# Kernel optimization log

Measured on AMD Instinct MI355X. Metric: run time of the kernel, lower is better.

The kernel has to match this reference:

```python
import jax, jax.numpy as jnp
import numpy as np

D_QK = 64

def _xavier(key, shape):
    # matches nn.init.xavier_uniform_ on (H, fan_in, fan_out)
    fan_in, fan_out = shape[-2], shape[-1]
    limit = float(np.sqrt(6.0 / (fan_in + fan_out)))
    return jax.random.uniform(key, shape, jnp.float32, -limit, limit)

def setup_inputs() -> dict:
    key = jax.random.key(0)
    kx, kq, kk, kv = jax.random.split(key, 4)
    B, M, d_model, H, d_QK, d_V = 4, 2048, 1024, 16, 64, 64
    x = jax.random.normal(kx, (B, M, d_model), jnp.float32)
    W_Q = _xavier(kq, (H, d_model, d_QK))
    W_K = _xavier(kk, (H, d_model, d_QK))
    W_V = _xavier(kv, (H, d_model, d_V))
    return {"x": x, "W_Q": W_Q, "W_K": W_K, "W_V": W_V}

def reference(x, W_Q, W_K, W_V):
    B, M, N = x.shape
    H = W_Q.shape[0]
    # per-head projections: [B,H,M,d]
    Q = jnp.einsum('bmn,hnd->bhmd', x, W_Q)
    K = jnp.einsum('bmn,hnd->bhmd', x, W_K)
    V = jnp.einsum('bmn,hnd->bhmd', x, W_V)
    scale = 1.0 / jnp.sqrt(jnp.asarray(D_QK, x.dtype))
    attn = jax.nn.softmax(jnp.einsum('bhmd,bhkd->bhmk', Q, K) * scale, axis=-1)
    out = jnp.einsum('bhmk,bhkd->bhmd', attn, V)  # [B,H,M,d_V]
    # transpose heads next to d_V and concat: [B,M,H*d_V] == [B,M,N]
    return out.transpose(0, 2, 1, 3).reshape(B, M, N)
```

## Files before the change

### kernel.cpp

```cpp
#include <hip/hip_runtime.h>

typedef __attribute__((ext_vector_type(8))) _Float16 f16x8;
typedef __attribute__((ext_vector_type(2))) __fp16 fp16v2;
typedef __attribute__((ext_vector_type(4))) float f32x4;
typedef _Float16 f16;
typedef unsigned short u16;
typedef unsigned int u32;

#define DEV __device__ __forceinline__

DEV u32 packh2(float a, float b) {
  union { f16 h[2]; u32 u; } x;
  x.h[0] = (f16)a; x.h[1] = (f16)b;
  return x.u;
}
DEV u32 pkrtz(float a, float b) {
  union { fp16v2 h; u32 u; } x;
  x.h = __builtin_amdgcn_cvt_pkrtz(a, b);
  return x.u;
}
DEV float exp2_fast(float x) {
  float r;
  asm("v_exp_f32 %0, %1" : "=v"(r) : "v"(x));
  return r;
}

typedef __attribute__((address_space(1))) const u32 ASG_u32;
typedef __attribute__((address_space(3))) u32 ASL_u32;
DEV void gload16(const void* g, void* l) {
  __builtin_amdgcn_global_load_lds((ASG_u32*)g, (ASL_u32*)l, 16, 0, 0);
}

__global__ __launch_bounds__(256) void k_half_x(const float* __restrict__ x,
                                                f16* __restrict__ xh) {
  const size_t i = ((size_t)blockIdx.x * 256 + threadIdx.x) * 8;
  float4 a = *(const float4*)(x + i);
  float4 c = *(const float4*)(x + i + 4);
  uint4 u;
  u.x = packh2(a.x, a.y); u.y = packh2(a.z, a.w);
  u.z = packh2(c.x, c.y); u.w = packh2(c.z, c.w);
  *(uint4*)(xh + i) = u;
}

__global__ __launch_bounds__(256) void k_prep_w(const float* __restrict__ Wq,
                                                const float* __restrict__ Wk,
                                                const float* __restrict__ Wv,
                                                f16* __restrict__ wt) {
  __shared__ float tile[64][65];
  const int bx = blockIdx.x;
  const int w = bx >> 8;
  const int rem = bx & 255;
  const int h = rem >> 4;
  const int nc = rem & 15;
  const float* W = (w == 0) ? Wq : ((w == 1) ? Wk : Wv);
  const int t = threadIdx.x;

  {
    const int r = t >> 2;
    const int cc = (t & 3) * 16;
    const float* src = W + ((size_t)h * 1024 + nc * 64 + r) * 64 + cc;
#pragma unroll
    for (int j = 0; j < 4; ++j) {
      float4 v = *(const float4*)(src + j * 4);
      tile[r][cc + j * 4 + 0] = v.x;
      tile[r][cc + j * 4 + 1] = v.y;
      tile[r][cc + j * 4 + 2] = v.z;
      tile[r][cc + j * 4 + 3] = v.w;
    }
  }
  __syncthreads();
  {
    const int d = t >> 2;
    const int n0 = (t & 3) * 16;
    const size_t base = ((size_t)(w * 16 + h) * 64 + d) * 1024 + nc * 64 + n0;
    uint4 u0, u1;
    u0.x = packh2(tile[n0 + 0][d], tile[n0 + 1][d]);
    u0.y = packh2(tile[n0 + 2][d], tile[n0 + 3][d]);
    u0.z = packh2(tile[n0 + 4][d], tile[n0 + 5][d]);
    u0.w = packh2(tile[n0 + 6][d], tile[n0 + 7][d]);
    u1.x = packh2(tile[n0 + 8][d], tile[n0 + 9][d]);
    u1.y = packh2(tile[n0 + 10][d], tile[n0 + 11][d]);
    u1.z = packh2(tile[n0 + 12][d], tile[n0 + 13][d]);
    u1.w = packh2(tile[n0 + 14][d], tile[n0 + 15][d]);
    *(uint4*)(wt + base) = u0;
    *(uint4*)(wt + base + 8) = u1;
  }
}

__global__ __launch_bounds__(256, 4) void k_proj(
    const f16* __restrict__ xh, const f16* __restrict__ wt,
    f16* __restrict__ Q, f16* __restrict__ K, f16* __restrict__ Vt) {
  __shared__ __align__(16) char ldsb[32768];
  int bid = blockIdx.x;
  bid = (bid & 7) * 192 + (bid >> 3);
  const int bm = bid / 24;
  const int bn = bid % 24;
  const int w = bn >> 3;
  const int hp = bn & 7;
  const int wrow = w * 1024 + hp * 128;
  const bool isV = (w == 2);
  const int t = threadIdx.x;
  const int wave = t >> 6;
  const int lane = t & 63;
  const int l15 = lane & 15;
  const int wr = wave >> 1;
  const int wc = wave & 1;

  f32x4 acc[4][4];
#pragma unroll
  for (int mi = 0; mi < 4; ++mi)
#pragma unroll
    for (int ni = 0; ni < 4; ++ni) acc[mi][ni] = (f32x4)(0.0f);

  for (int kt = 0; kt < 16; ++kt) {
    const int k0 = kt * 64;
#pragma unroll
    for (int i = 0; i < 4; ++i) {
      const int ci = wave * 4 + i;
      const int row = ci * 8 + (lane >> 3);
      const int cb = ((lane & 7) * 16) ^ ((row & 7) << 4);
      const size_t ga = ((size_t)(bm * 128 + row) * 1024 + k0) * 2;
      gload16((const char*)xh + ga + cb, ldsb + ci * 1024);
      const size_t gb = ((size_t)(wrow + row) * 1024 + k0) * 2;
      gload16((const char*)wt + gb + cb, ldsb + 16384 + ci * 1024);
    }
    __syncthreads();

#pragma unroll
    for (int ks = 0; ks < 2; ++ks) {
      f16x8 af[4], bfr[4];
#pragma unroll
      for (int mi = 0; mi < 4; ++mi) {
        const int row = wr * 64 + mi * 16 + l15;
        const int cb = (((lane >> 4) * 16) + ks * 64) ^ ((row & 7) << 4);
        af[mi] = *(const f16x8*)(ldsb + row * 128 + cb);
      }
#pragma unroll
      for (int ni = 0; ni < 4; ++ni) {
        const int row = wc * 64 + ni * 16 + l15;
        const int cb = (((lane >> 4) * 16) + ks * 64) ^ ((row & 7) << 4);
        bfr[ni] = *(const f16x8*)(ldsb + 16384 + row * 128 + cb);
      }
#pragma unroll
      for (int mi = 0; mi < 4; ++mi)
#pragma unroll
        for (int ni = 0; ni < 4; ++ni)
          acc[mi][ni] = __builtin_amdgcn_mfma_f32_16x16x32_f16(af[mi], bfr[ni], acc[mi][ni], 0, 0, 0);
    }
    __syncthreads();
  }

  const int rb = bm * 128 + wr * 64;
#pragma unroll
  for (int mi = 0; mi < 4; ++mi) {
#pragma unroll
    for (int ni = 0; ni < 4; ++ni) {
      f32x4 v = acc[mi][ni];
      const int dl = wc * 64 + ni * 16 + l15;
      const int hh = hp * 2 + (dl >> 6);
      const int d = dl & 63;
      const int m0 = rb + mi * 16 + ((lane >> 4) << 2);
      const int b = m0 >> 11;
      const int ml = m0 & 2047;
      if (isV) {
        uint2 u;
        u.x = packh2(v[0], v[1]);
        u.y = packh2(v[2], v[3]);
        *(uint2*)(Vt + ((size_t)((b * 16 + hh) * 64 + d)) * 2048 + ml) = u;
      } else {
        const float sc = (w == 0) ? 0.18033688f : 1.0f;
        f16* A = (w == 0) ? Q : K;
#pragma unroll
        for (int j = 0; j < 4; ++j)
          A[((size_t)(b * 16 + hh) * 2048 + (ml + j)) * 64 + d] = (f16)(v[j] * sc);
      }
    }
  }
}

__global__ __launch_bounds__(512, 4) void k_attn(
    const f16* __restrict__ Q, const f16* __restrict__ K,
    const f16* __restrict__ Vt, float* __restrict__ out) {
  __shared__ __align__(16) char ldsb[81920];
  const int raw = blockIdx.x;
  const int bh = (raw & 7) * 8 + (raw >> 6);
  const int qt = (raw >> 3) & 7;
  const int b = bh >> 4;
  const int h = bh & 15;
  const int t = threadIdx.x;
  const int wave = t >> 6;
  const int lane = t & 63;
  const int l15 = lane & 15;
  const int g = lane >> 4;
  char* sP = ldsb + 49152 + wave * 4096;

  f16x8 qf[2][2];
  const size_t qbase = ((size_t)bh * 2048 + qt * 256 + wave * 32) * 64;
#pragma unroll
  for (int mf = 0; mf < 2; ++mf)
#pragma unroll
    for (int ks = 0; ks < 2; ++ks) {
      const size_t off = qbase + (size_t)(mf * 16 + l15) * 64 + ks * 32 + g * 8;
      qf[mf][ks] = *(const f16x8*)(Q + off);
    }

  f32x4 o[2][4];
  float ms[2], ls[2];
#pragma unroll
  for (int mf = 0; mf < 2; ++mf) { ms[mf] = -1e30f; ls[mf] = 0.0f; }
#pragma unroll
  for (int mf = 0; mf < 2; ++mf)
#pragma unroll
    for (int df = 0; df < 4; ++df) o[mf][df] = (f32x4)(0.0f);

  const size_t kvbase = (size_t)bh * 2048 * 64;

  const int srow = wave * 8 + (lane >> 3);
  const int scb0 = ((lane & 7) * 16) ^ (((lane >> 3) & 7) << 4);

  auto stage = [&](int tile, int bufi) {
    char* dst = ldsb + bufi * 16384;
    const size_t gk = (kvbase + (size_t)(tile * 64 + srow) * 64) * 2;
    gload16((const char*)K + gk + scb0, dst + wave * 1024);
    const size_t gv = (kvbase + (size_t)srow * 2048 + tile * 64) * 2;
    gload16((const char*)Vt + gv + scb0, dst + 8192 + wave * 1024);
  };

  stage(0, 0);
  stage(1, 1);

  int cur = 0;
  int stg = 2;

#pragma unroll 1
  for (int ct = 0; ct < 32; ++ct) {
    if (ct < 31) {
      asm volatile("s_waitcnt vmcnt(2) lgkmcnt(0)" ::: "memory");
    } else {
      asm volatile("s_waitcnt vmcnt(0) lgkmcnt(0)" ::: "memory");
    }
    __builtin_amdgcn_s_barrier();
    __builtin_amdgcn_sched_barrier(0);

    if (ct + 2 < 32) stage(ct + 2, stg);

    const char* kb = ldsb + cur * 16384;
    const char* vbuf = kb + 8192;

    f32x4 st[2][4];
#pragma unroll
    for (int mf = 0; mf < 2; ++mf)
#pragma unroll
      for (int nf = 0; nf < 4; ++nf) st[mf][nf] = (f32x4)(0.0f);
#pragma unroll
    for (int ks = 0; ks < 2; ++ks) {
      f16x8 kf[4];
#pragma unroll
      for (int nf = 0; nf < 4; ++nf) {
        const int row = nf * 16 + l15;
        const int cb = ((g * 16) + ks * 64) ^ ((row & 7) << 4);
        kf[nf] = *(const f16x8*)(kb + row * 128 + cb);
      }
#pragma unroll
      for (int mf = 0; mf < 2; ++mf)
#pragma unroll
        for (int nf = 0; nf < 4; ++nf)
          st[mf][nf] = __builtin_amdgcn_mfma_f32_16x16x32_f16(kf[nf], qf[mf][ks], st[mf][nf], 0, 0, 0);
    }

#pragma unroll
    for (int mf = 0; mf < 2; ++mf) {
      float rm = fmaxf(fmaxf(fmaxf(st[mf][0][0], st[mf][0][1]), fmaxf(st[mf][0][2], st[mf][0][3])),
                       fmaxf(fmaxf(st[mf][1][0], st[mf][1][1]), fmaxf(st[mf][1][2], st[mf][1][3])));
      rm = fmaxf(rm, fmaxf(fmaxf(fmaxf(st[mf][2][0], st[mf][2][1]), fmaxf(st[mf][2][2], st[mf][2][3])),
                           fmaxf(fmaxf(st[mf][3][0], st[mf][3][1]), fmaxf(st[mf][3][2], st[mf][3][3]))));
      rm = fmaxf(rm, __shfl_xor(rm, 16));
      rm = fmaxf(rm, __shfl_xor(rm, 32));
      if (__any(rm > ms[mf] + 11.5f)) {
        const float mnew = fmaxf(ms[mf], rm);
        const float alpha = exp2_fast(ms[mf] - mnew);
        ms[mf] = mnew;
        ls[mf] *= alpha;
        f32x4 av;
#pragma unroll
        for (int j = 0; j < 4; ++j) av[j] = __shfl(alpha, g * 4 + j);
#pragma unroll
        for (int df = 0; df < 4; ++df) o[mf][df] *= av;
      }
      const float m = ms[mf];
      float p[4][4], part = 0.0f;
#pragma unroll
      for (int nf = 0; nf < 4; ++nf) {
#pragma unroll
        for (int j = 0; j < 4; ++j) {
          p[nf][j] = exp2_fast(st[mf][nf][j] - m);
          part += p[nf][j];
        }
      }
      ls[mf] += part;
      const int prow = mf * 16 + l15;
      char* pr = sP + prow * 128;
      const int swz = (prow & 7) << 4;
#pragma unroll
      for (int nf = 0; nf < 4; ++nf) {
        uint2 u;
        u.x = pkrtz(p[nf][0], p[nf][1]);
        u.y = pkrtz(p[nf][2], p[nf][3]);
        *(uint2*)(pr + (((nf << 5) + (g << 3)) ^ swz)) = u;
      }
    }
    asm volatile("" ::: "memory");

#pragma unroll
    for (int ks = 0; ks < 2; ++ks) {
      f16x8 pa[2];
#pragma unroll
      for (int mf = 0; mf < 2; ++mf) {
        const int prow = mf * 16 + l15;
        pa[mf] = *(const f16x8*)(sP + prow * 128 + ((ks * 64 + g * 16) ^ ((prow & 7) << 4)));
      }
#pragma unroll
      for (int df = 0; df < 4; ++df) {
        const int row = df * 16 + l15;
        const int cb = ((g * 16) + ks * 64) ^ ((row & 7) << 4);
        const f16x8 vb = *(const f16x8*)(vbuf + row * 128 + cb);
#pragma unroll
        for (int mf = 0; mf < 2; ++mf)
          o[mf][df] = __builtin_amdgcn_mfma_f32_16x16x32_f16(pa[mf], vb, o[mf][df], 0, 0, 0);
      }
    }

    cur = (cur == 2) ? 0 : cur + 1;
    stg = (stg == 2) ? 0 : stg + 1;
  }

#pragma unroll
  for (int mf = 0; mf < 2; ++mf) {
    float l = ls[mf];
    l += __shfl_xor(l, 16);
    l += __shfl_xor(l, 32);
    const float inv = 1.0f / l;
    f32x4 iv;
#pragma unroll
    for (int j = 0; j < 4; ++j) iv[j] = __shfl(inv, g * 4 + j);
#pragma unroll
    for (int j = 0; j < 4; ++j) {
      const int m = qt * 256 + wave * 32 + mf * 16 + g * 4 + j;
#pragma unroll
      for (int df = 0; df < 4; ++df) {
        const int d = df * 16 + l15;
        out[((size_t)(b * 2048 + m)) * 1024 + h * 64 + d] = o[mf][df][j] * iv[j];
      }
    }
  }
}

extern "C" void kernel_launch(void* const* d_in, const int* in_sizes, int n_in,
                              void* d_out, int out_size, void* d_ws, size_t ws_size,
                              hipStream_t stream) {
  (void)in_sizes; (void)n_in; (void)out_size; (void)ws_size;
  const float* x  = (const float*)d_in[0];
  const float* Wq = (const float*)d_in[1];
  const float* Wk = (const float*)d_in[2];
  const float* Wv = (const float*)d_in[3];
  float* out = (float*)d_out;

  f16* ws = (f16*)d_ws;
  f16* xh = ws + 0;
  f16* wt = ws + 8388608;
  f16* Q  = ws + 11534336;
  f16* K  = ws + 19922944;
  f16* Vt = ws + 28311552;

  k_half_x<<<4096, 256, 0, stream>>>(x, xh);
  k_prep_w<<<768, 256, 0, stream>>>(Wq, Wk, Wv, wt);
  k_proj<<<1536, 256, 0, stream>>>(xh, wt, Q, K, Vt);
  k_attn<<<512, 512, 0, stream>>>(Q, K, Vt, out);
}
```

Baseline: 183.1 us.

## Double per-wave query rows in attention and merge x/W prep kernels

The attention kernel now runs 4 waves per block, each handling 64 query rows instead of 32, with 8 waves before. Each K/V fragment read from LDS is reused across twice as many MFMAs, and each wave issues two async staging loads per tile. The x-to-half conversion and weight transpose kernels are merged into one launch to save a kernel launch. The cost is higher register pressure from doubled accumulators and fewer waves per block to hide latency.

```diff
diff --git a/kernel.cpp b/kernel.cpp
--- a/kernel.cpp
+++ b/kernel.cpp
@@ -31,29 +31,31 @@
   __builtin_amdgcn_global_load_lds((ASG_u32*)g, (ASL_u32*)l, 16, 0, 0);
 }
 
-__global__ __launch_bounds__(256) void k_half_x(const float* __restrict__ x,
-                                                f16* __restrict__ xh) {
-  const size_t i = ((size_t)blockIdx.x * 256 + threadIdx.x) * 8;
-  float4 a = *(const float4*)(x + i);
-  float4 c = *(const float4*)(x + i + 4);
-  uint4 u;
-  u.x = packh2(a.x, a.y); u.y = packh2(a.z, a.w);
-  u.z = packh2(c.x, c.y); u.w = packh2(c.z, c.w);
-  *(uint4*)(xh + i) = u;
-}
-
-__global__ __launch_bounds__(256) void k_prep_w(const float* __restrict__ Wq,
-                                                const float* __restrict__ Wk,
-                                                const float* __restrict__ Wv,
-                                                f16* __restrict__ wt) {
+__global__ __launch_bounds__(256) void k_pre(const float* __restrict__ x,
+                                             const float* __restrict__ Wq,
+                                             const float* __restrict__ Wk,
+                                             const float* __restrict__ Wv,
+                                             f16* __restrict__ xh,
+                                             f16* __restrict__ wt) {
   __shared__ float tile[64][65];
-  const int bx = blockIdx.x;
+  const int bx0 = blockIdx.x;
+  const int t = threadIdx.x;
+  if (bx0 < 4096) {
+    const size_t i = ((size_t)bx0 * 256 + t) * 8;
+    float4 a = *(const float4*)(x + i);
+    float4 c = *(const float4*)(x + i + 4);
+    uint4 u;
+    u.x = packh2(a.x, a.y); u.y = packh2(a.z, a.w);
+    u.z = packh2(c.x, c.y); u.w = packh2(c.z, c.w);
+    *(uint4*)(xh + i) = u;
+    return;
+  }
+  const int bx = bx0 - 4096;
   const int w = bx >> 8;
   const int rem = bx & 255;
   const int h = rem >> 4;
   const int nc = rem & 15;
   const float* W = (w == 0) ? Wq : ((w == 1) ? Wk : Wv);
-  const int t = threadIdx.x;
 
   {
     const int r = t >> 2;
@@ -178,7 +180,7 @@
   }
 }
 
-__global__ __launch_bounds__(512, 4) void k_attn(
+__global__ __launch_bounds__(256, 2) void k_attn(
     const f16* __restrict__ Q, const f16* __restrict__ K,
     const f16* __restrict__ Vt, float* __restrict__ out) {
   __shared__ __align__(16) char ldsb[81920];
@@ -192,38 +194,43 @@
   const int lane = t & 63;
   const int l15 = lane & 15;
   const int g = lane >> 4;
-  char* sP = ldsb + 49152 + wave * 4096;
-
-  f16x8 qf[2][2];
-  const size_t qbase = ((size_t)bh * 2048 + qt * 256 + wave * 32) * 64;
-#pragma unroll
-  for (int mf = 0; mf < 2; ++mf)
+  char* sP = ldsb + 49152 + wave * 8192;
+
+  f16x8 qf[4][2];
+  const size_t qbase = ((size_t)bh * 2048 + qt * 256 + wave * 64) * 64;
+#pragma unroll
+  for (int mf = 0; mf < 4; ++mf)
 #pragma unroll
     for (int ks = 0; ks < 2; ++ks) {
       const size_t off = qbase + (size_t)(mf * 16 + l15) * 64 + ks * 32 + g * 8;
       qf[mf][ks] = *(const f16x8*)(Q + off);
     }
 
-  f32x4 o[2][4];
-  float ms[2], ls[2];
-#pragma unroll
-  for (int mf = 0; mf < 2; ++mf) { ms[mf] = -1e30f; ls[mf] = 0.0f; }
-#pragma unroll
-  for (int mf = 0; mf < 2; ++mf)
+  f32x4 o[4][4];
+  float ms[4], ls[4];
+#pragma unroll
+  for (int mf = 0; mf < 4; ++mf) { ms[mf] = -1e30f; ls[mf] = 0.0f; }
+#pragma unroll
+  for (int mf = 0; mf < 4; ++mf)
 #pragma unroll
     for (int df = 0; df < 4; ++df) o[mf][df] = (f32x4)(0.0f);
 
   const size_t kvbase = (size_t)bh * 2048 * 64;
 
-  const int srow = wave * 8 + (lane >> 3);
-  const int scb0 = ((lane & 7) * 16) ^ (((lane >> 3) & 7) << 4);
+  const int srow = wave * 16 + (lane >> 3);
+  const int scb0 = ((lane & 7) * 16) ^ ((srow & 7) << 4);
 
   auto stage = [&](int tile, int bufi) {
     char* dst = ldsb + bufi * 16384;
-    const size_t gk = (kvbase + (size_t)(tile * 64 + srow) * 64) * 2;
-    gload16((const char*)K + gk + scb0, dst + wave * 1024);
-    const size_t gv = (kvbase + (size_t)srow * 2048 + tile * 64) * 2;
-    gload16((const char*)Vt + gv + scb0, dst + 8192 + wave * 1024);
+#pragma unroll
+    for (int i = 0; i < 2; ++i) {
+      const int ci = wave * 2 + i;
+      const int row = srow + i * 8;
+      const size_t gk = (kvbase + (size_t)(tile * 64 + row) * 64) * 2;
+      gload16((const char*)K + gk + scb0, dst + ci * 1024);
+      const size_t gv = (kvbase + (size_t)row * 2048 + tile * 64) * 2;
+      gload16((const char*)Vt + gv + scb0, dst + 8192 + ci * 1024);
+    }
   };
 
   stage(0, 0);
@@ -235,7 +242,7 @@
 #pragma unroll 1
   for (int ct = 0; ct < 32; ++ct) {
     if (ct < 31) {
-      asm volatile("s_waitcnt vmcnt(2) lgkmcnt(0)" ::: "memory");
+      asm volatile("s_waitcnt vmcnt(4) lgkmcnt(0)" ::: "memory");
     } else {
       asm volatile("s_waitcnt vmcnt(0) lgkmcnt(0)" ::: "memory");
     }
@@ -247,9 +254,9 @@
     const char* kb = ldsb + cur * 16384;
     const char* vbuf = kb + 8192;
 
-    f32x4 st[2][4];
-#pragma unroll
-    for (int mf = 0; mf < 2; ++mf)
+    f32x4 st[4][4];
+#pragma unroll
+    for (int mf = 0; mf < 4; ++mf)
 #pragma unroll
       for (int nf = 0; nf < 4; ++nf) st[mf][nf] = (f32x4)(0.0f);
 #pragma unroll
@@ -262,14 +269,14 @@
         kf[nf] = *(const f16x8*)(kb + row * 128 + cb);
       }
 #pragma unroll
-      for (int mf = 0; mf < 2; ++mf)
+      for (int mf = 0; mf < 4; ++mf)
 #pragma unroll
         for (int nf = 0; nf < 4; ++nf)
           st[mf][nf] = __builtin_amdgcn_mfma_f32_16x16x32_f16(kf[nf], qf[mf][ks], st[mf][nf], 0, 0, 0);
     }
 
 #pragma unroll
-    for (int mf = 0; mf < 2; ++mf) {
+    for (int mf = 0; mf < 4; ++mf) {
       float rm = fmaxf(fmaxf(fmaxf(st[mf][0][0], st[mf][0][1]), fmaxf(st[mf][0][2], st[mf][0][3])),
                        fmaxf(fmaxf(st[mf][1][0], st[mf][1][1]), fmaxf(st[mf][1][2], st[mf][1][3])));
       rm = fmaxf(rm, fmaxf(fmaxf(fmaxf(st[mf][2][0], st[mf][2][1]), fmaxf(st[mf][2][2], st[mf][2][3])),
@@ -313,9 +320,9 @@
 
 #pragma unroll
     for (int ks = 0; ks < 2; ++ks) {
-      f16x8 pa[2];
-#pragma unroll
-      for (int mf = 0; mf < 2; ++mf) {
+      f16x8 pa[4];
+#pragma unroll
+      for (int mf = 0; mf < 4; ++mf) {
         const int prow = mf * 16 + l15;
         pa[mf] = *(const f16x8*)(sP + prow * 128 + ((ks * 64 + g * 16) ^ ((prow & 7) << 4)));
       }
@@ -325,7 +332,7 @@
         const int cb = ((g * 16) + ks * 64) ^ ((row & 7) << 4);
         const f16x8 vb = *(const f16x8*)(vbuf + row * 128 + cb);
 #pragma unroll
-        for (int mf = 0; mf < 2; ++mf)
+        for (int mf = 0; mf < 4; ++mf)
           o[mf][df] = __builtin_amdgcn_mfma_f32_16x16x32_f16(pa[mf], vb, o[mf][df], 0, 0, 0);
       }
     }
@@ -335,7 +342,7 @@
   }
 
 #pragma unroll
-  for (int mf = 0; mf < 2; ++mf) {
+  for (int mf = 0; mf < 4; ++mf) {
     float l = ls[mf];
     l += __shfl_xor(l, 16);
     l += __shfl_xor(l, 32);
@@ -345,7 +352,7 @@
     for (int j = 0; j < 4; ++j) iv[j] = __shfl(inv, g * 4 + j);
 #pragma unroll
     for (int j = 0; j < 4; ++j) {
-      const int m = qt * 256 + wave * 32 + mf * 16 + g * 4 + j;
+      const int m = qt * 256 + wave * 64 + mf * 16 + g * 4 + j;
 #pragma unroll
       for (int df = 0; df < 4; ++df) {
         const int d = df * 16 + l15;
@@ -372,8 +379,7 @@
   f16* K  = ws + 19922944;
   f16* Vt = ws + 28311552;
 
-  k_half_x<<<4096, 256, 0, stream>>>(x, xh);
-  k_prep_w<<<768, 256, 0, stream>>>(Wq, Wk, Wv, wt);
+  k_pre<<<4864, 256, 0, stream>>>(x, Wq, Wk, Wv, xh, wt);
   k_proj<<<1536, 256, 0, stream>>>(xh, wt, Q, K, Vt);
-  k_attn<<<512, 512, 0, stream>>>(Q, K, Vt, out);
-}
+  k_attn<<<512, 256, 0, stream>>>(Q, K, Vt, out);
+}
```

After: 183.0 us. About the same (-0.0%).

## Software-pipeline QK of next tile with softmax/PV of current; merge prep kernels

Applied to the files above, without the earlier changes.

The attention loop is restructured so the QK^T MFMAs for tile ct+1 are issued before the softmax and PV of tile ct, using two alternating score register sets. All three LDS buffers are prefetched up front, and each refill is issued after a barrier once its buffer is consumed. This is meant to hide softmax latency behind matrix work. The x-to-half and weight-prep kernels are merged into one launch to save a kernel launch, and the attention launch bound is lowered to 2 blocks so the extra live registers fit, at some cost in occupancy.

```diff
diff --git a/kernel.cpp b/kernel.cpp
--- a/kernel.cpp
+++ b/kernel.cpp
@@ -31,29 +31,31 @@
   __builtin_amdgcn_global_load_lds((ASG_u32*)g, (ASL_u32*)l, 16, 0, 0);
 }
 
-__global__ __launch_bounds__(256) void k_half_x(const float* __restrict__ x,
-                                                f16* __restrict__ xh) {
-  const size_t i = ((size_t)blockIdx.x * 256 + threadIdx.x) * 8;
-  float4 a = *(const float4*)(x + i);
-  float4 c = *(const float4*)(x + i + 4);
-  uint4 u;
-  u.x = packh2(a.x, a.y); u.y = packh2(a.z, a.w);
-  u.z = packh2(c.x, c.y); u.w = packh2(c.z, c.w);
-  *(uint4*)(xh + i) = u;
-}
-
-__global__ __launch_bounds__(256) void k_prep_w(const float* __restrict__ Wq,
-                                                const float* __restrict__ Wk,
-                                                const float* __restrict__ Wv,
-                                                f16* __restrict__ wt) {
+__global__ __launch_bounds__(256) void k_pre(const float* __restrict__ x,
+                                             const float* __restrict__ Wq,
+                                             const float* __restrict__ Wk,
+                                             const float* __restrict__ Wv,
+                                             f16* __restrict__ xh,
+                                             f16* __restrict__ wt) {
   __shared__ float tile[64][65];
-  const int bx = blockIdx.x;
+  const int bx0 = blockIdx.x;
+  const int t = threadIdx.x;
+  if (bx0 < 4096) {
+    const size_t i = ((size_t)bx0 * 256 + t) * 8;
+    float4 a = *(const float4*)(x + i);
+    float4 c = *(const float4*)(x + i + 4);
+    uint4 u;
+    u.x = packh2(a.x, a.y); u.y = packh2(a.z, a.w);
+    u.z = packh2(c.x, c.y); u.w = packh2(c.z, c.w);
+    *(uint4*)(xh + i) = u;
+    return;
+  }
+  const int bx = bx0 - 4096;
   const int w = bx >> 8;
   const int rem = bx & 255;
   const int h = rem >> 4;
   const int nc = rem & 15;
   const float* W = (w == 0) ? Wq : ((w == 1) ? Wk : Wv);
-  const int t = threadIdx.x;
 
   {
     const int r = t >> 2;
@@ -178,7 +180,7 @@
   }
 }
 
-__global__ __launch_bounds__(512, 4) void k_attn(
+__global__ __launch_bounds__(512, 2) void k_attn(
     const f16* __restrict__ Q, const f16* __restrict__ K,
     const f16* __restrict__ Vt, float* __restrict__ out) {
   __shared__ __align__(16) char ldsb[81920];
@@ -226,28 +228,8 @@
     gload16((const char*)Vt + gv + scb0, dst + 8192 + wave * 1024);
   };
 
-  stage(0, 0);
-  stage(1, 1);
-
-  int cur = 0;
-  int stg = 2;
-
-#pragma unroll 1
-  for (int ct = 0; ct < 32; ++ct) {
-    if (ct < 31) {
-      asm volatile("s_waitcnt vmcnt(2) lgkmcnt(0)" ::: "memory");
-    } else {
-      asm volatile("s_waitcnt vmcnt(0) lgkmcnt(0)" ::: "memory");
-    }
-    __builtin_amdgcn_s_barrier();
-    __builtin_amdgcn_sched_barrier(0);
-
-    if (ct + 2 < 32) stage(ct + 2, stg);
-
-    const char* kb = ldsb + cur * 16384;
-    const char* vbuf = kb + 8192;
-
-    f32x4 st[2][4];
+  auto qk = [&](int tile, f32x4 (&st)[2][4]) {
+    const char* kb = ldsb + (tile % 3) * 16384;
 #pragma unroll
     for (int mf = 0; mf < 2; ++mf)
 #pragma unroll
@@ -267,7 +249,10 @@
         for (int nf = 0; nf < 4; ++nf)
           st[mf][nf] = __builtin_amdgcn_mfma_f32_16x16x32_f16(kf[nf], qf[mf][ks], st[mf][nf], 0, 0, 0);
     }
-
+  };
+
+  auto smpv = [&](int ct, f32x4 (&st)[2][4]) {
+    const char* vbuf = ldsb + (ct % 3) * 16384 + 8192;
 #pragma unroll
     for (int mf = 0; mf < 2; ++mf) {
       float rm = fmaxf(fmaxf(fmaxf(st[mf][0][0], st[mf][0][1]), fmaxf(st[mf][0][2], st[mf][0][3])),
@@ -329,9 +314,50 @@
           o[mf][df] = __builtin_amdgcn_mfma_f32_16x16x32_f16(pa[mf], vb, o[mf][df], 0, 0, 0);
       }
     }
-
-    cur = (cur == 2) ? 0 : cur + 1;
-    stg = (stg == 2) ? 0 : stg + 1;
+  };
+
+  stage(0, 0);
+  stage(1, 1);
+  stage(2, 2);
+  asm volatile("s_waitcnt vmcnt(4) lgkmcnt(0)" ::: "memory");
+  __builtin_amdgcn_s_barrier();
+  __builtin_amdgcn_sched_barrier(0);
+
+  f32x4 stA[2][4], stB[2][4];
+  qk(0, stA);
+
+#pragma unroll 1
+  for (int c2 = 0; c2 < 32; c2 += 2) {
+    {
+      const int ct = c2;
+      if (ct < 30) {
+        asm volatile("s_waitcnt vmcnt(2) lgkmcnt(0)" ::: "memory");
+      } else {
+        asm volatile("s_waitcnt vmcnt(0) lgkmcnt(0)" ::: "memory");
+      }
+      __builtin_amdgcn_s_barrier();
+      __builtin_amdgcn_sched_barrier(0);
+      qk(ct + 1, stB);
+      smpv(ct, stA);
+      __builtin_amdgcn_s_barrier();
+      if (ct + 3 < 32) stage(ct + 3, ct % 3);
+    }
+    {
+      const int ct = c2 + 1;
+      if (ct < 31) {
+        if (ct < 30) {
+          asm volatile("s_waitcnt vmcnt(2) lgkmcnt(0)" ::: "memory");
+        } else {
+          asm volatile("s_waitcnt vmcnt(0) lgkmcnt(0)" ::: "memory");
+        }
+        __builtin_amdgcn_s_barrier();
+        __builtin_amdgcn_sched_barrier(0);
+        qk(ct + 1, stA);
+      }
+      smpv(ct, stB);
+      __builtin_amdgcn_s_barrier();
+      if (ct + 3 < 32) stage(ct + 3, ct % 3);
+    }
   }
 
 #pragma unroll
@@ -372,8 +398,7 @@
   f16* K  = ws + 19922944;
   f16* Vt = ws + 28311552;
 
-  k_half_x<<<4096, 256, 0, stream>>>(x, xh);
-  k_prep_w<<<768, 256, 0, stream>>>(Wq, Wk, Wv, wt);
+  k_pre<<<4864, 256, 0, stream>>>(x, Wq, Wk, Wv, xh, wt);
   k_proj<<<1536, 256, 0, stream>>>(xh, wt, Q, K, Vt);
   k_attn<<<512, 512, 0, stream>>>(Q, K, Vt, out);
 }
```

New measurement: 190.4 us. 4.0% more time.
